# Kernel tuning notes

Hardware: AMD Instinct MI355X
Metric: run time of the kernel (lower is better)

The kernel has to match this reference:

```python
import jax, jax.numpy as jnp
import numpy as np

N_CLS = 1000
FEAT_DIM = 1024
BATCH = 32768
PROTO_M = 0.95
TEMP = 0.1
BASE_TEMP = 0.1


def setup_inputs() -> dict:
    key = jax.random.key(0)
    k1, k2, k3 = jax.random.split(key, 3)
    features = jax.random.normal(k1, (BATCH, FEAT_DIM), dtype=jnp.float32)
    labels = jax.random.randint(k2, (BATCH,), 0, N_CLS)
    p = jax.random.normal(k3, (N_CLS, FEAT_DIM), dtype=jnp.float32)
    prototypes = p / jnp.maximum(jnp.linalg.norm(p, axis=1, keepdims=True), 1e-12)
    return {"features": features, "prototypes": prototypes, "labels": labels}


def _l2_normalize(x, eps=1e-12):
    # F.normalize(x, dim=0) semantics: x / max(||x||_2, eps)
    return x / jnp.maximum(jnp.linalg.norm(x), eps)


def _ema_update(prototypes, features, labels):
    # Sequential per-sample EMA + renormalize (faithful to the torch for-loop:
    # later samples with the same label see earlier updates).
    def step(protos, fl):
        f, l = fl
        row = _l2_normalize(protos[l] * PROTO_M + f * (1.0 - PROTO_M))
        return protos.at[l].set(row), None

    prototypes, _ = jax.lax.scan(step, prototypes, (features, labels))
    return prototypes


def reference(features, prototypes, labels):
    protos = _ema_update(prototypes, features, labels)  # [n_cls, feat]
    logits = jnp.matmul(protos, protos.T) / TEMP        # [n_cls, n_cls]
    # mask = (1 - eye) * logits_mask, where logits_mask also zeros the diagonal
    mask = 1.0 - jnp.eye(N_CLS, dtype=logits.dtype)
    mean_prob_neg = jnp.log((mask * jnp.exp(logits)).sum(axis=1) / mask.sum(axis=1))
    # torch drops NaNs; with n_cls > 1 every row has n_cls-1 negatives, so none occur
    loss = (TEMP / BASE_TEMP) * jnp.mean(mean_prob_neg)
    return loss
```

## Files before the change

### kernel.cpp

```cpp
#include <hip/hip_runtime.h>
#include <math.h>

#define N_CLS 1000
#define FEAT  1024
#define BATCH 32768
#define NBLK_H 128
#define CHUNK  256

__global__ __launch_bounds__(256) void hist_kernel(const int* __restrict__ labels,
                                                   unsigned* __restrict__ hist) {
    __shared__ unsigned cnt[N_CLS];
    const int t = threadIdx.x, b = blockIdx.x;
    for (int i = t; i < N_CLS; i += 256) cnt[i] = 0;
    __syncthreads();
    const int l = labels[b * CHUNK + t];
    atomicAdd(&cnt[l], 1u);
    __syncthreads();
    for (int i = t; i < N_CLS; i += 256) hist[(size_t)b * N_CLS + i] = cnt[i];
}

__global__ __launch_bounds__(1024) void offsets_kernel(unsigned* __restrict__ hist,
                                                       unsigned* __restrict__ base,
                                                       unsigned* __restrict__ total) {
    const int t = threadIdx.x;
    unsigned run = 0;
    if (t < N_CLS) {
        for (int b = 0; b < NBLK_H; ++b) {
            unsigned v = hist[(size_t)b * N_CLS + t];
            hist[(size_t)b * N_CLS + t] = run;
            run += v;
        }
        total[t] = run;
    }
    __shared__ unsigned sc[1024];
    sc[t] = (t < N_CLS) ? run : 0u;
    __syncthreads();
    for (int off = 1; off < 1024; off <<= 1) {
        unsigned v = sc[t];
        unsigned u = (t >= off) ? sc[t - off] : 0u;
        __syncthreads();
        sc[t] = v + u;
        __syncthreads();
    }
    if (t < N_CLS) base[t] = sc[t] - run;
}

__global__ __launch_bounds__(256) void scatter_kernel(const int* __restrict__ labels,
                                                      const unsigned* __restrict__ hist,
                                                      const unsigned* __restrict__ base,
                                                      int* __restrict__ sorted_idx) {
    __shared__ int lbl[CHUNK];
    const int t = threadIdx.x, b = blockIdx.x;
    const int i = b * CHUNK + t;
    const int l = labels[i];
    lbl[t] = l;
    __syncthreads();
    int rank = 0;
    for (int j = 0; j < t; ++j) rank += (lbl[j] == l);
    const unsigned pos = base[l] + hist[(size_t)b * N_CLS + l] + (unsigned)rank;
    sorted_idx[pos] = i;
}

__device__ __forceinline__ float4 ema4(float4 p, float4 f) {
    p.x = fmaf(0.95f, p.x, 0.05f * f.x);
    p.y = fmaf(0.95f, p.y, 0.05f * f.y);
    p.z = fmaf(0.95f, p.z, 0.05f * f.z);
    p.w = fmaf(0.95f, p.w, 0.05f * f.w);
    return p;
}
__device__ __forceinline__ float dot4(float4 a) {
    return a.x * a.x + a.y * a.y + a.z * a.z + a.w * a.w;
}
__device__ __forceinline__ float4 scale4(float4 a, float s) {
    a.x *= s; a.y *= s; a.z *= s; a.w *= s; return a;
}

__global__ __launch_bounds__(256) void ema_kernel(const float* __restrict__ features,
                                                  const float* __restrict__ prototypes,
                                                  const int* __restrict__ sorted_idx,
                                                  const unsigned* __restrict__ base,
                                                  const unsigned* __restrict__ total,
                                                  float* __restrict__ protos_new) {
    const int w    = blockIdx.x * 4 + (threadIdx.x >> 6);
    const int lane = threadIdx.x & 63;
    const float4* pr = (const float4*)(prototypes + (size_t)w * FEAT);
    float4 p0 = pr[lane], p1 = pr[lane + 64], p2 = pr[lane + 128], p3 = pr[lane + 192];

    const int cnt = (int)total[w];
    const int bs  = (int)base[w];
    int sidx = (cnt > 0) ? sorted_idx[bs] : 0;
    for (int k = 0; k < cnt; ++k) {
        const float4* fr = (const float4*)(features + (size_t)sidx * FEAT);
        float4 f0 = fr[lane], f1 = fr[lane + 64], f2 = fr[lane + 128], f3 = fr[lane + 192];
        int nidx = (k + 1 < cnt) ? sorted_idx[bs + k + 1] : 0;
        p0 = ema4(p0, f0); p1 = ema4(p1, f1); p2 = ema4(p2, f2); p3 = ema4(p3, f3);
        float ss = dot4(p0) + dot4(p1) + dot4(p2) + dot4(p3);
        #pragma unroll
        for (int off = 32; off; off >>= 1) ss += __shfl_xor(ss, off, 64);
        const float inv = 1.0f / fmaxf(sqrtf(ss), 1e-12f);
        p0 = scale4(p0, inv); p1 = scale4(p1, inv); p2 = scale4(p2, inv); p3 = scale4(p3, inv);
        sidx = nidx;
    }
    float4* out = (float4*)(protos_new + (size_t)w * FEAT);
    out[lane] = p0; out[lane + 64] = p1; out[lane + 128] = p2; out[lane + 192] = p3;
}

#define BM 64
#define BN 32
#define BK 32

__global__ __launch_bounds__(256) void gram_kernel(const float* __restrict__ P,
                                                   float* __restrict__ S) {
    __shared__ float As[BK][BM + 2];
    __shared__ float Bs[BK][BN + 4];
    const int t  = threadIdx.x;
    const int bx = blockIdx.x;
    const int by = blockIdx.y;
    const int tc = t & 7;
    const int tr = t >> 3;
    const int c0 = tc * 4, r0 = tr * 2;

    float acc[2][4] = {{0.f,0.f,0.f,0.f},{0.f,0.f,0.f,0.f}};

    const int la_r = t >> 3;
    const int la_k = (t & 7) * 4;

    for (int k0 = 0; k0 < FEAT; k0 += BK) {
        #pragma unroll
        for (int h = 0; h < 2; ++h) {
            const int r  = la_r + h * 32;
            const int gr = by * BM + r;
            float4 v = make_float4(0.f, 0.f, 0.f, 0.f);
            if (gr < N_CLS) v = *(const float4*)(P + (size_t)gr * FEAT + k0 + la_k);
            As[la_k + 0][r] = v.x; As[la_k + 1][r] = v.y;
            As[la_k + 2][r] = v.z; As[la_k + 3][r] = v.w;
        }
        {
            const int gc = bx * BN + la_r;
            float4 v = make_float4(0.f, 0.f, 0.f, 0.f);
            if (gc < N_CLS) v = *(const float4*)(P + (size_t)gc * FEAT + k0 + la_k);
            Bs[la_k + 0][la_r] = v.x; Bs[la_k + 1][la_r] = v.y;
            Bs[la_k + 2][la_r] = v.z; Bs[la_k + 3][la_r] = v.w;
        }
        __syncthreads();
        #pragma unroll
        for (int k = 0; k < BK; ++k) {
            const float a0 = As[k][r0], a1 = As[k][r0 + 1];
            const float b0 = Bs[k][c0], b1 = Bs[k][c0 + 1];
            const float b2 = Bs[k][c0 + 2], b3 = Bs[k][c0 + 3];
            acc[0][0] = fmaf(a0, b0, acc[0][0]); acc[0][1] = fmaf(a0, b1, acc[0][1]);
            acc[0][2] = fmaf(a0, b2, acc[0][2]); acc[0][3] = fmaf(a0, b3, acc[0][3]);
            acc[1][0] = fmaf(a1, b0, acc[1][0]); acc[1][1] = fmaf(a1, b1, acc[1][1]);
            acc[1][2] = fmaf(a1, b2, acc[1][2]); acc[1][3] = fmaf(a1, b3, acc[1][3]);
        }
        __syncthreads();
    }

    float rs[2];
    #pragma unroll
    for (int i = 0; i < 2; ++i) {
        const int gr = by * BM + r0 + i;
        float s = 0.f;
        #pragma unroll
        for (int j = 0; j < 4; ++j) {
            const int gc = bx * BN + c0 + j;
            if (gr < N_CLS && gc < N_CLS && gr != gc) s += expf(acc[i][j] * 10.0f);
        }
        rs[i] = s;
    }
    #pragma unroll
    for (int m = 1; m < 8; m <<= 1) {
        rs[0] += __shfl_xor(rs[0], m, 64);
        rs[1] += __shfl_xor(rs[1], m, 64);
    }
    if (tc == 0) {
        #pragma unroll
        for (int i = 0; i < 2; ++i) {
            const int gr = by * BM + r0 + i;
            if (gr < N_CLS) atomicAdd(&S[gr], rs[i]);
        }
    }
}

__global__ __launch_bounds__(1024) void loss_kernel(const float* __restrict__ S,
                                                    float* __restrict__ out) {
    const int t = threadIdx.x;
    float v = 0.f;
    if (t < N_CLS) v = logf(S[t]) - logf(999.0f);
    #pragma unroll
    for (int off = 32; off; off >>= 1) v += __shfl_xor(v, off, 64);
    __shared__ float red[16];
    const int wv = t >> 6, lane = t & 63;
    if (lane == 0) red[wv] = v;
    __syncthreads();
    if (t < 16) {
        float s = red[t];
        #pragma unroll
        for (int off = 8; off; off >>= 1) s += __shfl_xor(s, off, 16);
        if (t == 0) out[0] = s / (float)N_CLS;
    }
}

extern "C" void kernel_launch(void* const* d_in, const int* in_sizes, int n_in,
                              void* d_out, int out_size, void* d_ws, size_t ws_size,
                              hipStream_t stream) {
    const float* features   = (const float*)d_in[0];
    const float* prototypes = (const float*)d_in[1];
    const int*   labels     = (const int*)d_in[2];
    float* out = (float*)d_out;

    char* ws = (char*)d_ws;
    unsigned* hist   = (unsigned*)(ws);
    unsigned* base   = (unsigned*)(ws + 512000);
    unsigned* total  = (unsigned*)(ws + 516096);
    int*      sorted = (int*)     (ws + 520192);
    float*    pnew   = (float*)   (ws + 651264);
    float*    S      = (float*)   (ws + 651264 + 4096000);

    hist_kernel   <<<NBLK_H, 256, 0, stream>>>(labels, hist);
    offsets_kernel<<<1, 1024, 0, stream>>>(hist, base, total);
    scatter_kernel<<<NBLK_H, 256, 0, stream>>>(labels, hist, base, sorted);
    ema_kernel    <<<250, 256, 0, stream>>>(features, prototypes, sorted, base, total, pnew);
    hipMemsetAsync(S, 0, N_CLS * sizeof(float), stream);
    gram_kernel   <<<dim3(32, 16), 256, 0, stream>>>(pnew, S);
    loss_kernel   <<<1, 1024, 0, stream>>>(S, out);
}
```

Measured before the change: 298.7 us.

## Use split-bf16 MFMA Gram, parallel histogram scan, and double-buffered EMA loads

```diff
diff --git a/kernel.cpp b/kernel.cpp
--- a/kernel.cpp
+++ b/kernel.cpp
@@ -1,4 +1,5 @@
 #include <hip/hip_runtime.h>
+#include <hip/hip_bf16.h>
 #include <math.h>
 
 #define N_CLS 1000
@@ -6,6 +7,23 @@
 #define BATCH 32768
 #define NBLK_H 128
 #define CHUNK  256
+#define KCAT   3072
+#define GBK    64
+#define LPITCH 72
+
+typedef short short8 __attribute__((ext_vector_type(8)));
+typedef float f32x4  __attribute__((ext_vector_type(4)));
+
+__device__ __forceinline__ unsigned short f2bf(float x) {
+    union { __hip_bfloat16 h; unsigned short u; } cv;
+    cv.h = __float2bfloat16(x);
+    return cv.u;
+}
+__device__ __forceinline__ float bf2f(unsigned short u) {
+    union { __hip_bfloat16 h; unsigned short u; } cv;
+    cv.u = u;
+    return __bfloat162float(cv.h);
+}
 
 __global__ __launch_bounds__(256) void hist_kernel(const int* __restrict__ labels,
                                                    unsigned* __restrict__ hist) {
@@ -13,36 +31,45 @@
     const int t = threadIdx.x, b = blockIdx.x;
     for (int i = t; i < N_CLS; i += 256) cnt[i] = 0;
     __syncthreads();
-    const int l = labels[b * CHUNK + t];
-    atomicAdd(&cnt[l], 1u);
-    __syncthreads();
-    for (int i = t; i < N_CLS; i += 256) hist[(size_t)b * N_CLS + i] = cnt[i];
-}
-
-__global__ __launch_bounds__(1024) void offsets_kernel(unsigned* __restrict__ hist,
-                                                       unsigned* __restrict__ base,
-                                                       unsigned* __restrict__ total) {
+    atomicAdd(&cnt[labels[b * CHUNK + t]], 1u);
+    __syncthreads();
+    for (int i = t; i < N_CLS; i += 256) hist[(size_t)i * NBLK_H + b] = cnt[i];
+}
+
+__global__ __launch_bounds__(256) void scan1_kernel(unsigned* __restrict__ hist,
+                                                    unsigned* __restrict__ total) {
+    const int l    = blockIdx.x * 4 + (threadIdx.x >> 6);
+    const int lane = threadIdx.x & 63;
+    unsigned v0 = hist[(size_t)l * NBLK_H + lane];
+    unsigned v1 = hist[(size_t)l * NBLK_H + 64 + lane];
+    unsigned x0 = v0, x1 = v1;
+    #pragma unroll
+    for (int off = 1; off < 64; off <<= 1) {
+        unsigned u0 = __shfl_up(x0, off, 64);
+        if (lane >= off) x0 += u0;
+        unsigned u1 = __shfl_up(x1, off, 64);
+        if (lane >= off) x1 += u1;
+    }
+    x1 += __shfl(x0, 63, 64);
+    hist[(size_t)l * NBLK_H + lane]      = x0 - v0;
+    hist[(size_t)l * NBLK_H + 64 + lane] = x1 - v1;
+    if (lane == 63) total[l] = x1;
+}
+
+__global__ __launch_bounds__(1024) void scan2_kernel(const unsigned* __restrict__ total,
+                                                     unsigned* __restrict__ base) {
     const int t = threadIdx.x;
-    unsigned run = 0;
-    if (t < N_CLS) {
-        for (int b = 0; b < NBLK_H; ++b) {
-            unsigned v = hist[(size_t)b * N_CLS + t];
-            hist[(size_t)b * N_CLS + t] = run;
-            run += v;
-        }
-        total[t] = run;
-    }
+    unsigned v = (t < N_CLS) ? total[t] : 0u;
     __shared__ unsigned sc[1024];
-    sc[t] = (t < N_CLS) ? run : 0u;
+    sc[t] = v;
     __syncthreads();
     for (int off = 1; off < 1024; off <<= 1) {
-        unsigned v = sc[t];
         unsigned u = (t >= off) ? sc[t - off] : 0u;
         __syncthreads();
-        sc[t] = v + u;
-        __syncthreads();
-    }
-    if (t < N_CLS) base[t] = sc[t] - run;
+        sc[t] += u;
+        __syncthreads();
+    }
+    if (t < N_CLS) base[t] = sc[t] - v;
 }
 
 __global__ __launch_bounds__(256) void scatter_kernel(const int* __restrict__ labels,
@@ -50,15 +77,20 @@
                                                       const unsigned* __restrict__ base,
                                                       int* __restrict__ sorted_idx) {
     __shared__ int lbl[CHUNK];
+    __shared__ unsigned c[N_CLS];
     const int t = threadIdx.x, b = blockIdx.x;
+    for (int i = t; i < N_CLS; i += 256) c[i] = 0;
+    __syncthreads();
     const int i = b * CHUNK + t;
     const int l = labels[i];
     lbl[t] = l;
+    atomicAdd(&c[l], 1u);
     __syncthreads();
     int rank = 0;
-    for (int j = 0; j < t; ++j) rank += (lbl[j] == l);
-    const unsigned pos = base[l] + hist[(size_t)b * N_CLS + l] + (unsigned)rank;
-    sorted_idx[pos] = i;
+    if (c[l] > 1) {
+        for (int j = 0; j < t; ++j) rank += (lbl[j] == l);
+    }
+    sorted_idx[base[l] + hist[(size_t)l * NBLK_H + b] + (unsigned)rank] = i;
 }
 
 __device__ __forceinline__ float4 ema4(float4 p, float4 f) {
@@ -88,96 +120,132 @@
 
     const int cnt = (int)total[w];
     const int bs  = (int)base[w];
-    int sidx = (cnt > 0) ? sorted_idx[bs] : 0;
-    for (int k = 0; k < cnt; ++k) {
-        const float4* fr = (const float4*)(features + (size_t)sidx * FEAT);
-        float4 f0 = fr[lane], f1 = fr[lane + 64], f2 = fr[lane + 128], f3 = fr[lane + 192];
-        int nidx = (k + 1 < cnt) ? sorted_idx[bs + k + 1] : 0;
-        p0 = ema4(p0, f0); p1 = ema4(p1, f1); p2 = ema4(p2, f2); p3 = ema4(p3, f3);
+    const int iA = (cnt > 0) ? sorted_idx[bs] : 0;
+    const int iB = (cnt > 1) ? sorted_idx[bs + 1] : 0;
+    const float4* fA = (const float4*)(features + (size_t)iA * FEAT);
+    float4 a0 = fA[lane], a1 = fA[lane + 64], a2 = fA[lane + 128], a3 = fA[lane + 192];
+    const float4* fB = (const float4*)(features + (size_t)iB * FEAT);
+    float4 b0 = fB[lane], b1 = fB[lane + 64], b2 = fB[lane + 128], b3 = fB[lane + 192];
+
+    int k = 0;
+    while (k + 2 <= cnt) {
+        {
+            const int iN = (k + 2 < cnt) ? sorted_idx[bs + k + 2] : 0;
+            p0 = ema4(p0, a0); p1 = ema4(p1, a1); p2 = ema4(p2, a2); p3 = ema4(p3, a3);
+            const float4* f = (const float4*)(features + (size_t)iN * FEAT);
+            a0 = f[lane]; a1 = f[lane + 64]; a2 = f[lane + 128]; a3 = f[lane + 192];
+            float ss = dot4(p0) + dot4(p1) + dot4(p2) + dot4(p3);
+            #pragma unroll
+            for (int o = 32; o; o >>= 1) ss += __shfl_xor(ss, o, 64);
+            const float inv = 1.0f / fmaxf(sqrtf(ss), 1e-12f);
+            p0 = scale4(p0, inv); p1 = scale4(p1, inv); p2 = scale4(p2, inv); p3 = scale4(p3, inv);
+        }
+        {
+            const int iN = (k + 3 < cnt) ? sorted_idx[bs + k + 3] : 0;
+            p0 = ema4(p0, b0); p1 = ema4(p1, b1); p2 = ema4(p2, b2); p3 = ema4(p3, b3);
+            const float4* f = (const float4*)(features + (size_t)iN * FEAT);
+            b0 = f[lane]; b1 = f[lane + 64]; b2 = f[lane + 128]; b3 = f[lane + 192];
+            float ss = dot4(p0) + dot4(p1) + dot4(p2) + dot4(p3);
+            #pragma unroll
+            for (int o = 32; o; o >>= 1) ss += __shfl_xor(ss, o, 64);
+            const float inv = 1.0f / fmaxf(sqrtf(ss), 1e-12f);
+            p0 = scale4(p0, inv); p1 = scale4(p1, inv); p2 = scale4(p2, inv); p3 = scale4(p3, inv);
+        }
+        k += 2;
+    }
+    if (k < cnt) {
+        p0 = ema4(p0, a0); p1 = ema4(p1, a1); p2 = ema4(p2, a2); p3 = ema4(p3, a3);
         float ss = dot4(p0) + dot4(p1) + dot4(p2) + dot4(p3);
         #pragma unroll
-        for (int off = 32; off; off >>= 1) ss += __shfl_xor(ss, off, 64);
+        for (int o = 32; o; o >>= 1) ss += __shfl_xor(ss, o, 64);
         const float inv = 1.0f / fmaxf(sqrtf(ss), 1e-12f);
         p0 = scale4(p0, inv); p1 = scale4(p1, inv); p2 = scale4(p2, inv); p3 = scale4(p3, inv);
-        sidx = nidx;
     }
     float4* out = (float4*)(protos_new + (size_t)w * FEAT);
     out[lane] = p0; out[lane + 64] = p1; out[lane + 128] = p2; out[lane + 192] = p3;
 }
 
-#define BM 64
-#define BN 32
-#define BK 32
-
-__global__ __launch_bounds__(256) void gram_kernel(const float* __restrict__ P,
+__global__ __launch_bounds__(256) void convert_kernel(const float* __restrict__ P,
+                                                      unsigned short* __restrict__ A,
+                                                      unsigned short* __restrict__ Bm) {
+    const int row = blockIdx.x;
+    const int t   = threadIdx.x;
+    float4 v = make_float4(0.f, 0.f, 0.f, 0.f);
+    if (row < N_CLS) v = *(const float4*)(P + (size_t)row * FEAT + 4 * t);
+    ushort4 hi, lo;
+    hi.x = f2bf(v.x); lo.x = f2bf(v.x - bf2f(hi.x));
+    hi.y = f2bf(v.y); lo.y = f2bf(v.y - bf2f(hi.y));
+    hi.z = f2bf(v.z); lo.z = f2bf(v.z - bf2f(hi.z));
+    hi.w = f2bf(v.w); lo.w = f2bf(v.w - bf2f(hi.w));
+    const size_t rb = (size_t)row * KCAT;
+    *(ushort4*)(A  + rb +        4 * t) = hi;
+    *(ushort4*)(A  + rb + 1024 + 4 * t) = lo;
+    *(ushort4*)(A  + rb + 2048 + 4 * t) = hi;
+    *(ushort4*)(Bm + rb +        4 * t) = hi;
+    *(ushort4*)(Bm + rb + 1024 + 4 * t) = hi;
+    *(ushort4*)(Bm + rb + 2048 + 4 * t) = lo;
+}
+
+__global__ __launch_bounds__(256) void gram_kernel(const unsigned short* __restrict__ A,
+                                                   const unsigned short* __restrict__ Bm,
                                                    float* __restrict__ S) {
-    __shared__ float As[BK][BM + 2];
-    __shared__ float Bs[BK][BN + 4];
-    const int t  = threadIdx.x;
-    const int bx = blockIdx.x;
-    const int by = blockIdx.y;
-    const int tc = t & 7;
-    const int tr = t >> 3;
-    const int c0 = tc * 4, r0 = tr * 2;
-
-    float acc[2][4] = {{0.f,0.f,0.f,0.f},{0.f,0.f,0.f,0.f}};
-
-    const int la_r = t >> 3;
-    const int la_k = (t & 7) * 4;
-
-    for (int k0 = 0; k0 < FEAT; k0 += BK) {
-        #pragma unroll
-        for (int h = 0; h < 2; ++h) {
-            const int r  = la_r + h * 32;
-            const int gr = by * BM + r;
-            float4 v = make_float4(0.f, 0.f, 0.f, 0.f);
-            if (gr < N_CLS) v = *(const float4*)(P + (size_t)gr * FEAT + k0 + la_k);
-            As[la_k + 0][r] = v.x; As[la_k + 1][r] = v.y;
-            As[la_k + 2][r] = v.z; As[la_k + 3][r] = v.w;
-        }
-        {
-            const int gc = bx * BN + la_r;
-            float4 v = make_float4(0.f, 0.f, 0.f, 0.f);
-            if (gc < N_CLS) v = *(const float4*)(P + (size_t)gc * FEAT + k0 + la_k);
-            Bs[la_k + 0][la_r] = v.x; Bs[la_k + 1][la_r] = v.y;
-            Bs[la_k + 2][la_r] = v.z; Bs[la_k + 3][la_r] = v.w;
-        }
-        __syncthreads();
-        #pragma unroll
-        for (int k = 0; k < BK; ++k) {
-            const float a0 = As[k][r0], a1 = As[k][r0 + 1];
-            const float b0 = Bs[k][c0], b1 = Bs[k][c0 + 1];
-            const float b2 = Bs[k][c0 + 2], b3 = Bs[k][c0 + 3];
-            acc[0][0] = fmaf(a0, b0, acc[0][0]); acc[0][1] = fmaf(a0, b1, acc[0][1]);
-            acc[0][2] = fmaf(a0, b2, acc[0][2]); acc[0][3] = fmaf(a0, b3, acc[0][3]);
-            acc[1][0] = fmaf(a1, b0, acc[1][0]); acc[1][1] = fmaf(a1, b1, acc[1][1]);
-            acc[1][2] = fmaf(a1, b2, acc[1][2]); acc[1][3] = fmaf(a1, b3, acc[1][3]);
-        }
-        __syncthreads();
-    }
-
-    float rs[2];
+    __shared__ short As[64 * LPITCH];
+    __shared__ short Bs[64 * LPITCH];
+    const int t = threadIdx.x;
+    const int l = t & 63, wid = t >> 6;
+    const int wr = wid >> 1, wc = wid & 1;
+    const int m0 = blockIdx.y * 64, n0 = blockIdx.x * 64;
+    const int lg = l >> 4, lc = l & 15;
+
+    f32x4 acc[2][2] = {};
+
+    const int r0s = t >> 3,          c0s = t & 7;
+    const int r1s = (t + 256) >> 3,  c1s = t & 7;
+    const short* Ag = (const short*)A;
+    const short* Bg = (const short*)Bm;
+
+    for (int k0 = 0; k0 < KCAT; k0 += GBK) {
+        short8 a0 = *(const short8*)(Ag + (size_t)(m0 + r0s) * KCAT + k0 + c0s * 8);
+        short8 a1 = *(const short8*)(Ag + (size_t)(m0 + r1s) * KCAT + k0 + c1s * 8);
+        short8 g0 = *(const short8*)(Bg + (size_t)(n0 + r0s) * KCAT + k0 + c0s * 8);
+        short8 g1 = *(const short8*)(Bg + (size_t)(n0 + r1s) * KCAT + k0 + c1s * 8);
+        __syncthreads();
+        *(short8*)(As + r0s * LPITCH + c0s * 8) = a0;
+        *(short8*)(As + r1s * LPITCH + c1s * 8) = a1;
+        *(short8*)(Bs + r0s * LPITCH + c0s * 8) = g0;
+        *(short8*)(Bs + r1s * LPITCH + c1s * 8) = g1;
+        __syncthreads();
+        #pragma unroll
+        for (int kk = 0; kk < 2; ++kk) {
+            short8 af[2], bf[2];
+            #pragma unroll
+            for (int mi = 0; mi < 2; ++mi)
+                af[mi] = *(const short8*)(As + (wr * 32 + mi * 16 + lc) * LPITCH + kk * 32 + lg * 8);
+            #pragma unroll
+            for (int ni = 0; ni < 2; ++ni)
+                bf[ni] = *(const short8*)(Bs + (wc * 32 + ni * 16 + lc) * LPITCH + kk * 32 + lg * 8);
+            #pragma unroll
+            for (int mi = 0; mi < 2; ++mi)
+                #pragma unroll
+                for (int ni = 0; ni < 2; ++ni)
+                    acc[mi][ni] = __builtin_amdgcn_mfma_f32_16x16x32_bf16(af[mi], bf[ni], acc[mi][ni], 0, 0, 0);
+        }
+    }
+
     #pragma unroll
-    for (int i = 0; i < 2; ++i) {
-        const int gr = by * BM + r0 + i;
-        float s = 0.f;
+    for (int mi = 0; mi < 2; ++mi) {
         #pragma unroll
         for (int j = 0; j < 4; ++j) {
-            const int gc = bx * BN + c0 + j;
-            if (gr < N_CLS && gc < N_CLS && gr != gc) s += expf(acc[i][j] * 10.0f);
-        }
-        rs[i] = s;
-    }
-    #pragma unroll
-    for (int m = 1; m < 8; m <<= 1) {
-        rs[0] += __shfl_xor(rs[0], m, 64);
-        rs[1] += __shfl_xor(rs[1], m, 64);
-    }
-    if (tc == 0) {
-        #pragma unroll
-        for (int i = 0; i < 2; ++i) {
-            const int gr = by * BM + r0 + i;
-            if (gr < N_CLS) atomicAdd(&S[gr], rs[i]);
+            const int gr = m0 + wr * 32 + mi * 16 + lg * 4 + j;
+            float s = 0.f;
+            #pragma unroll
+            for (int ni = 0; ni < 2; ++ni) {
+                const int gc = n0 + wc * 32 + ni * 16 + lc;
+                if (gr < N_CLS && gc < N_CLS && gr != gc) s += expf(acc[mi][ni][j] * 10.0f);
+            }
+            #pragma unroll
+            for (int m = 1; m < 16; m <<= 1) s += __shfl_xor(s, m, 64);
+            if (lc == 0 && gr < N_CLS) atomicAdd(&S[gr], s);
         }
     }
 }
@@ -210,18 +278,22 @@
     float* out = (float*)d_out;
 
     char* ws = (char*)d_ws;
-    unsigned* hist   = (unsigned*)(ws);
-    unsigned* base   = (unsigned*)(ws + 512000);
-    unsigned* total  = (unsigned*)(ws + 516096);
-    int*      sorted = (int*)     (ws + 520192);
-    float*    pnew   = (float*)   (ws + 651264);
-    float*    S      = (float*)   (ws + 651264 + 4096000);
+    unsigned*       hist   = (unsigned*)(ws);
+    unsigned*       base   = (unsigned*)(ws + 0x80000);
+    unsigned*       total  = (unsigned*)(ws + 0x81000);
+    int*            sorted = (int*)     (ws + 0x82000);
+    float*          S      = (float*)   (ws + 0xA4000);
+    float*          pnew   = (float*)   (ws + 0x100000);
+    unsigned short* Acat   = (unsigned short*)(ws + 0x500000);
+    unsigned short* Bcat   = (unsigned short*)(ws + 0xB00000);
 
     hist_kernel   <<<NBLK_H, 256, 0, stream>>>(labels, hist);
-    offsets_kernel<<<1, 1024, 0, stream>>>(hist, base, total);
+    scan1_kernel  <<<250, 256, 0, stream>>>(hist, total);
+    scan2_kernel  <<<1, 1024, 0, stream>>>(total, base);
     scatter_kernel<<<NBLK_H, 256, 0, stream>>>(labels, hist, base, sorted);
+    hipMemsetAsync(S, 0, N_CLS * sizeof(float), stream);
     ema_kernel    <<<250, 256, 0, stream>>>(features, prototypes, sorted, base, total, pnew);
-    hipMemsetAsync(S, 0, N_CLS * sizeof(float), stream);
-    gram_kernel   <<<dim3(32, 16), 256, 0, stream>>>(pnew, S);
+    convert_kernel<<<1024, 256, 0, stream>>>(pnew, Acat, Bcat);
+    gram_kernel   <<<dim3(16, 16), 256, 0, stream>>>(Acat, Bcat, S);
     loss_kernel   <<<1, 1024, 0, stream>>>(S, out);
 }
```

After: 265.4 us. -11.1%, faster.
